# Optimization experiments

Measured on AMD Instinct MI355X. Metric: run time of the kernel, lower is better.

Reference implementation:

```python
import jax, jax.numpy as jnp
import numpy as np

B = 65536
HIDDEN = 200
K = 10          # num codewords == codeword dim (NearestEmbed(k, emb_size=k))
GROUPS = HIDDEN // K  # 20 sub-vectors of dim K per sample


def setup_inputs() -> dict:
    key = jax.random.key(0)
    ks = jax.random.split(key, 10)
    s = 0.05  # small init scale
    return {
        "x": jax.random.uniform(ks[0], (B, 784), dtype=jnp.float32),
        "W1": jax.random.normal(ks[1], (400, 784), dtype=jnp.float32) * s,
        "b1": jnp.zeros((400,), dtype=jnp.float32),
        "W2": jax.random.normal(ks[2], (HIDDEN, 400), dtype=jnp.float32) * s,
        "b2": jnp.zeros((HIDDEN,), dtype=jnp.float32),
        "W3": jax.random.normal(ks[3], (400, HIDDEN), dtype=jnp.float32) * s,
        "b3": jnp.zeros((400,), dtype=jnp.float32),
        "W4": jax.random.normal(ks[4], (784, 400), dtype=jnp.float32) * s,
        "b4": jnp.zeros((784,), dtype=jnp.float32),
        "codebook": jax.random.normal(ks[5], (K, K), dtype=jnp.float32),  # (n_codes, code_dim)
    }


def _quantize(z, codebook):
    # z: (B, K, GROUPS) -- quantize each length-K column vector to nearest codeword.
    v = jnp.transpose(z, (0, 2, 1))                       # (B, G, K)
    d2 = (jnp.sum(v * v, -1, keepdims=True)
          - 2.0 * jnp.einsum('bgk,ck->bgc', v, codebook)
          + jnp.sum(codebook * codebook, -1))             # (B, G, C)
    idx = jnp.argmin(d2, axis=-1)                         # (B, G)
    q = codebook[idx]                                     # (B, G, K) gather
    return jnp.transpose(q, (0, 2, 1)), idx               # (B, K, G)


def reference(x, W1, b1, W2, b2, W3, b3, W4, b4, codebook):
    # encode
    h1 = jax.nn.relu(x @ W1.T + b1)                       # (B, 400)
    z_e_flat = h1 @ W2.T + b2                             # (B, 200)
    z_e = z_e_flat.reshape(B, K, GROUPS)                  # (B, 10, 20)

    # z_q: straight-through quantization, codebook grad stopped (weight_sg=True)
    q, _ = _quantize(z_e, codebook)
    z_q = (z_e + jax.lax.stop_gradient(q - z_e)).reshape(B, HIDDEN)

    # emb: quantize detached z_e; gradient flows only to codebook via gather
    q2, _ = _quantize(jax.lax.stop_gradient(z_e), codebook)
    emb = q2.reshape(B, HIDDEN)

    # decode (original uses tanh on the output)
    h3 = jax.nn.relu(z_q @ W3.T + b3)                     # (B, 400)
    recon = jnp.tanh(h3 @ W4.T + b4)                      # (B, 784)
    return recon, z_e, emb
```

## Files before the change

### kernel.cpp

```cpp
#include <hip/hip_runtime.h>
#include <hip/hip_bf16.h>

#define NB   65536
#define KD   10
#define NG   20
#define NH   200
#define NH1  400
#define NIN  784

#define TAU 3e-4

using short8 = __attribute__((ext_vector_type(8))) short;
using f32x4  = __attribute__((ext_vector_type(4))) float;

__device__ inline float bf2f(unsigned short u) {
  union { unsigned int i; float f; } x; x.i = ((unsigned int)u) << 16; return x.f;
}
__device__ inline unsigned short f2bf(float v) {
  __hip_bfloat16 b = __float2bfloat16(v);
  return *reinterpret_cast<unsigned short*>(&b);
}
__device__ inline void split2(float v, unsigned short& h, unsigned short& l) {
  union { float f; unsigned int i; } u; u.f = v;
  const unsigned int hbits = u.i & 0xffff0000u;
  h = (unsigned short)(hbits >> 16);
  union { unsigned int i; float f; } w; w.i = hbits;
  l = f2bf(v - w.f);
}
__device__ inline void gload_lds16(const void* g, void* l) {
  __builtin_amdgcn_global_load_lds(
      (const __attribute__((address_space(1))) unsigned int*)g,
      (__attribute__((address_space(3))) unsigned int*)l, 16, 0, 0);
}

#define KSWZ(lane) ((((lane) & 3) ^ (((lane) >> 3) & 3)) * 8)
#define CSW(lane)  (((((lane) >> 4) ^ (((lane) >> 1) & 3))) * 8)

__global__ __launch_bounds__(512) void gemm1_fused(
    const float* __restrict__ xf,
    const unsigned short* __restrict__ Bhi, const unsigned short* __restrict__ Blo,
    const float* __restrict__ bias,
    unsigned short* __restrict__ Ohi, unsigned short* __restrict__ Olo)
{
  __shared__ __align__(16) short As_hi[2][128][32];
  __shared__ __align__(16) short As_lo[2][128][32];
  __shared__ __align__(16) short Bs_hi[2][128][32];
  __shared__ __align__(16) short Bs_lo[2][128][32];
  const int tid = threadIdx.x;
  const int lane = tid & 63, wid = tid >> 6;
  const int wr = wid >> 2, wc = wid & 3;
  const int bid = blockIdx.x;
  const int sw = (bid & 7) * 256 + (bid >> 3);
  const int n0 = (sw & 3) * 128;
  const int m0 = (sw >> 2) * 128;
  const int rr = lane >> 2;
  const int kswz = KSWZ(lane);
  const int csw = CSW(lane);
  const int fr = lane & 15;
  const int arow = tid >> 3;
  const int wbyte = ((tid & 7) * 8) ^ (((tid >> 4) & 3) << 4);
  const int acol = (tid & 7) * 4;

  f32x4 acc[4][2];
  #pragma unroll
  for (int i = 0; i < 4; ++i)
    #pragma unroll
    for (int j = 0; j < 2; ++j) acc[i][j] = (f32x4){0.f, 0.f, 0.f, 0.f};

  float4 va0, va1;

  auto loadA = [&](int ks) {
    const int k0 = ks * 32;
    const int kk = k0 + acol;
    va0 = make_float4(0.f, 0.f, 0.f, 0.f);
    va1 = va0;
    if (kk < NIN) {
      va0 = *reinterpret_cast<const float4*>(xf + (size_t)(m0 + arow) * NIN + kk);
      va1 = *reinterpret_cast<const float4*>(xf + (size_t)(m0 + 64 + arow) * NIN + kk);
    }
  };
  auto stageB = [&](int ks, int buf) {
    const int k0 = ks * 32;
    #pragma unroll
    for (int c = 0; c < 2; ++c) {
      const int ch = wid * 2 + c;
      if (ch < 8)
        gload_lds16(Bhi + (size_t)(n0 + ch * 16 + rr) * 800 + k0 + kswz,
                    (char*)&Bs_hi[buf][0][0] + ch * 1024);
      else
        gload_lds16(Blo + (size_t)(n0 + (ch - 8) * 16 + rr) * 800 + k0 + kswz,
                    (char*)&Bs_lo[buf][0][0] + (ch - 8) * 1024);
    }
  };
  auto writeA = [&](int buf) {
    char* bh = (char*)&As_hi[buf][0][0];
    char* bl = (char*)&As_lo[buf][0][0];
    short4 h, l;
    split2(va0.x, (unsigned short&)h.x, (unsigned short&)l.x);
    split2(va0.y, (unsigned short&)h.y, (unsigned short&)l.y);
    split2(va0.z, (unsigned short&)h.z, (unsigned short&)l.z);
    split2(va0.w, (unsigned short&)h.w, (unsigned short&)l.w);
    *reinterpret_cast<short4*>(bh + arow * 64 + wbyte) = h;
    *reinterpret_cast<short4*>(bl + arow * 64 + wbyte) = l;
    split2(va1.x, (unsigned short&)h.x, (unsigned short&)l.x);
    split2(va1.y, (unsigned short&)h.y, (unsigned short&)l.y);
    split2(va1.z, (unsigned short&)h.z, (unsigned short&)l.z);
    split2(va1.w, (unsigned short&)h.w, (unsigned short&)l.w);
    *reinterpret_cast<short4*>(bh + (64 + arow) * 64 + wbyte) = h;
    *reinterpret_cast<short4*>(bl + (64 + arow) * 64 + wbyte) = l;
  };

  stageB(0, 0);
  loadA(0);
  writeA(0);
  __syncthreads();

  for (int ks = 0; ks < 25; ++ks) {
    const int cur = ks & 1, nxt = cur ^ 1;
    const bool more = (ks + 1 < 25);
    if (more) {
      stageB(ks + 1, nxt);
      loadA(ks + 1);
    }
    short8 ah[4], al[4], bh[2], bl[2];
    #pragma unroll
    for (int i = 0; i < 4; ++i) {
      ah[i] = *reinterpret_cast<const short8*>(&As_hi[cur][wr * 64 + i * 16 + fr][csw]);
      al[i] = *reinterpret_cast<const short8*>(&As_lo[cur][wr * 64 + i * 16 + fr][csw]);
    }
    #pragma unroll
    for (int j = 0; j < 2; ++j) {
      bh[j] = *reinterpret_cast<const short8*>(&Bs_hi[cur][wc * 32 + j * 16 + fr][csw]);
      bl[j] = *reinterpret_cast<const short8*>(&Bs_lo[cur][wc * 32 + j * 16 + fr][csw]);
    }
    #pragma unroll
    for (int i = 0; i < 4; ++i)
      #pragma unroll
      for (int j = 0; j < 2; ++j) {
        acc[i][j] = __builtin_amdgcn_mfma_f32_16x16x32_bf16(ah[i], bh[j], acc[i][j], 0, 0, 0);
        acc[i][j] = __builtin_amdgcn_mfma_f32_16x16x32_bf16(al[i], bh[j], acc[i][j], 0, 0, 0);
        acc[i][j] = __builtin_amdgcn_mfma_f32_16x16x32_bf16(ah[i], bl[j], acc[i][j], 0, 0, 0);
      }
    if (more) writeA(nxt);
    __syncthreads();
  }

  #pragma unroll
  for (int j = 0; j < 2; ++j) {
    const int n = n0 + wc * 32 + j * 16 + (lane & 15);
    if (n >= NH1) continue;
    const float bn = bias[n];
    #pragma unroll
    for (int i = 0; i < 4; ++i) {
      const int mb = m0 + wr * 64 + i * 16 + (lane >> 4) * 4;
      #pragma unroll
      for (int r = 0; r < 4; ++r) {
        float v = fmaxf(acc[i][j][r] + bn, 0.f);
        unsigned short h, l;
        split2(v, h, l);
        Ohi[(size_t)(mb + r) * NH1 + n] = h;
        Olo[(size_t)(mb + r) * NH1 + n] = l;
      }
    }
  }
}

__global__ __launch_bounds__(256) void gemm2_split(
    const unsigned short* __restrict__ Ahi, const unsigned short* __restrict__ Alo,
    const unsigned short* __restrict__ Bhi, const unsigned short* __restrict__ Blo,
    const unsigned short* __restrict__ zp, const float* __restrict__ bias,
    float* __restrict__ Of)
{
  __shared__ __align__(16) short As_hi[128][32];
  __shared__ __align__(16) short As_lo[128][32];
  __shared__ __align__(16) short Bs_hi[128][32];
  __shared__ __align__(16) short Bs_lo[128][32];
  const int tid = threadIdx.x;
  const int lane = tid & 63, wid = tid >> 6;
  const int wr = wid >> 1, wc = wid & 1;
  const int bid = blockIdx.x;
  const int sw = (bid & 7) * 128 + (bid >> 3);
  const int n0 = (sw & 1) * 128;
  const int m0 = (sw >> 1) * 128;

  const unsigned short* G = (wid == 0) ? Ahi : (wid == 1) ? Alo
                          : (wid == 2) ? Bhi : Blo;
  short* Lt = (wid == 0) ? &As_hi[0][0] : (wid == 1) ? &As_lo[0][0]
            : (wid == 2) ? &Bs_hi[0][0] : &Bs_lo[0][0];
  const bool isA = wid < 2;
  const int rbase = isA ? m0 : n0;
  const int ld = isA ? 400 : 416;
  const int rr = lane >> 2;
  const int kswz = KSWZ(lane);
  const int csw = CSW(lane);

  f32x4 acc[4][4];
  #pragma unroll
  for (int i = 0; i < 4; ++i)
    #pragma unroll
    for (int j = 0; j < 4; ++j) acc[i][j] = (f32x4){0.f, 0.f, 0.f, 0.f};

  for (int ks = 0; ks < 13; ++ks) {
    const int k0 = ks * 32;
    #pragma unroll
    for (int c = 0; c < 8; ++c) {
      const unsigned short* src =
          G + (size_t)(rbase + c * 16 + rr) * ld + k0 + kswz;
      if (isA && (k0 + kswz >= 400)) src = zp;
      gload_lds16(src, (char*)Lt + c * 1024);
    }
    __syncthreads();
    short8 ah[4], al[4], bh[4], bl[4];
    #pragma unroll
    for (int i = 0; i < 4; ++i) {
      ah[i] = *reinterpret_cast<const short8*>(&As_hi[wr * 64 + i * 16 + (lane & 15)][csw]);
      al[i] = *reinterpret_cast<const short8*>(&As_lo[wr * 64 + i * 16 + (lane & 15)][csw]);
      bh[i] = *reinterpret_cast<const short8*>(&Bs_hi[wc * 64 + i * 16 + (lane & 15)][csw]);
      bl[i] = *reinterpret_cast<const short8*>(&Bs_lo[wc * 64 + i * 16 + (lane & 15)][csw]);
    }
    #pragma unroll
    for (int i = 0; i < 4; ++i)
      #pragma unroll
      for (int j = 0; j < 4; ++j) {
        acc[i][j] = __builtin_amdgcn_mfma_f32_16x16x32_bf16(ah[i], bh[j], acc[i][j], 0, 0, 0);
        acc[i][j] = __builtin_amdgcn_mfma_f32_16x16x32_bf16(al[i], bh[j], acc[i][j], 0, 0, 0);
        acc[i][j] = __builtin_amdgcn_mfma_f32_16x16x32_bf16(ah[i], bl[j], acc[i][j], 0, 0, 0);
      }
    __syncthreads();
  }

  #pragma unroll
  for (int j = 0; j < 4; ++j) {
    const int n = n0 + wc * 64 + j * 16 + (lane & 15);
    if (n >= NH) continue;
    const float bn = bias[n];
    #pragma unroll
    for (int i = 0; i < 4; ++i) {
      const int mb = m0 + wr * 64 + i * 16 + (lane >> 4) * 4;
      #pragma unroll
      for (int r = 0; r < 4; ++r)
        Of[(size_t)(mb + r) * NH + n] = acc[i][j][r] + bn;
    }
  }
}

__global__ __launch_bounds__(512) void gemm3_mfma(
    const unsigned short* __restrict__ A,
    const __hip_bfloat16* __restrict__ Bp,
    const float* __restrict__ bias, __hip_bfloat16* __restrict__ H3)
{
  __shared__ __align__(16) short As[2][128][32];
  __shared__ __align__(16) short Bs[2][128][32];
  const int tid = threadIdx.x;
  const int lane = tid & 63, wid = tid >> 6;
  const int wr = wid >> 2, wc = wid & 3;
  const int bid = blockIdx.x;
  const int sw = (bid & 7) * 256 + (bid >> 3);
  const int n0 = (sw & 3) * 128;
  const int m0 = (sw >> 2) * 128;
  const int rr = lane >> 2;
  const int kswz = KSWZ(lane);
  const int csw = CSW(lane);
  const int fr = lane & 15;
  const short* Ag = (const short*)A;
  const short* Bg = (const short*)Bp;

  f32x4 acc[4][2];
  #pragma unroll
  for (int i = 0; i < 4; ++i)
    #pragma unroll
    for (int j = 0; j < 2; ++j) acc[i][j] = (f32x4){0.f, 0.f, 0.f, 0.f};

  auto stage = [&](int ks, int buf) {
    const int k0 = ks * 32;
    #pragma unroll
    for (int c = 0; c < 2; ++c) {
      const int ch = wid * 2 + c;
      if (ch < 8)
        gload_lds16(Ag + (size_t)(m0 + ch * 16 + rr) * 200 + k0 + kswz,
                    (char*)&As[buf][0][0] + ch * 1024);
      else
        gload_lds16(Bg + (size_t)(n0 + (ch - 8) * 16 + rr) * 224 + k0 + kswz,
                    (char*)&Bs[buf][0][0] + (ch - 8) * 1024);
    }
  };

  stage(0, 0);
  __syncthreads();
  for (int ks = 0; ks < 7; ++ks) {
    const int cur = ks & 1;
    if (ks + 1 < 7) stage(ks + 1, cur ^ 1);
    short8 af[4], bf[2];
    #pragma unroll
    for (int i = 0; i < 4; ++i)
      af[i] = *reinterpret_cast<const short8*>(&As[cur][wr * 64 + i * 16 + fr][csw]);
    #pragma unroll
    for (int j = 0; j < 2; ++j)
      bf[j] = *reinterpret_cast<const short8*>(&Bs[cur][wc * 32 + j * 16 + fr][csw]);
    #pragma unroll
    for (int i = 0; i < 4; ++i)
      #pragma unroll
      for (int j = 0; j < 2; ++j)
        acc[i][j] = __builtin_amdgcn_mfma_f32_16x16x32_bf16(af[i], bf[j], acc[i][j], 0, 0, 0);
    __syncthreads();
  }

  #pragma unroll
  for (int j = 0; j < 2; ++j) {
    const int n = n0 + wc * 32 + j * 16 + (lane & 15);
    if (n >= NH1) continue;
    const float bn = bias[n];
    #pragma unroll
    for (int i = 0; i < 4; ++i) {
      const int mb = m0 + wr * 64 + i * 16 + (lane >> 4) * 4;
      #pragma unroll
      for (int r = 0; r < 4; ++r)
        H3[(size_t)(mb + r) * NH1 + n] = __float2bfloat16(fmaxf(acc[i][j][r] + bn, 0.f));
    }
  }
}

__global__ __launch_bounds__(512) void gemm5_mfma(
    const __hip_bfloat16* __restrict__ A,
    const __hip_bfloat16* __restrict__ Bp,
    const float* __restrict__ bias, float* __restrict__ C)
{
  __shared__ __align__(16) short As[2][128][32];
  __shared__ __align__(16) short Bs[2][128][32];
  const int tid = threadIdx.x;
  const int lane = tid & 63, wid = tid >> 6;
  const int wr = wid >> 2, wc = wid & 3;
  const int bid = blockIdx.x;
  const int sw = (bid & 7) * 448 + (bid >> 3);
  const int n0 = (sw % 7) * 128;
  const int m0 = (sw / 7) * 128;
  const int rr = lane >> 2;
  const int kswz = KSWZ(lane);
  const int csw = CSW(lane);
  const int fr = lane & 15;
  const short* Ag = (const short*)A;
  const short* Bg = (const short*)Bp;

  f32x4 acc[4][2];
  #pragma unroll
  for (int i = 0; i < 4; ++i)
    #pragma unroll
    for (int j = 0; j < 2; ++j) acc[i][j] = (f32x4){0.f, 0.f, 0.f, 0.f};

  auto stage = [&](int ks, int buf) {
    const int k0 = ks * 32;
    #pragma unroll
    for (int c = 0; c < 2; ++c) {
      const int ch = wid * 2 + c;
      if (ch < 8)
        gload_lds16(Ag + (size_t)(m0 + ch * 16 + rr) * 400 + k0 + kswz,
                    (char*)&As[buf][0][0] + ch * 1024);
      else
        gload_lds16(Bg + (size_t)(n0 + (ch - 8) * 16 + rr) * 416 + k0 + kswz,
                    (char*)&Bs[buf][0][0] + (ch - 8) * 1024);
    }
  };

  stage(0, 0);
  __syncthreads();
  for (int ks = 0; ks < 13; ++ks) {
    const int cur = ks & 1;
    if (ks + 1 < 13) stage(ks + 1, cur ^ 1);
    short8 af[4], bf[2];
    #pragma unroll
    for (int i = 0; i < 4; ++i)
      af[i] = *reinterpret_cast<const short8*>(&As[cur][wr * 64 + i * 16 + fr][csw]);
    #pragma unroll
    for (int j = 0; j < 2; ++j)
      bf[j] = *reinterpret_cast<const short8*>(&Bs[cur][wc * 32 + j * 16 + fr][csw]);
    #pragma unroll
    for (int i = 0; i < 4; ++i)
      #pragma unroll
      for (int j = 0; j < 2; ++j)
        acc[i][j] = __builtin_amdgcn_mfma_f32_16x16x32_bf16(af[i], bf[j], acc[i][j], 0, 0, 0);
    __syncthreads();
  }

  #pragma unroll
  for (int j = 0; j < 2; ++j) {
    const int n = n0 + wc * 32 + j * 16 + (lane & 15);
    if (n >= NIN) continue;
    const float bn = bias[n];
    #pragma unroll
    for (int i = 0; i < 4; ++i) {
      const int mb = m0 + wr * 64 + i * 16 + (lane >> 4) * 4;
      #pragma unroll
      for (int r = 0; r < 4; ++r) {
        const float zv = acc[i][j][r] + bn;
        const float t = __expf(2.0f * zv);
        C[(size_t)(mb + r) * NIN + n] = 1.0f - __fdividef(2.0f, t + 1.0f);
      }
    }
  }
}

__global__ __launch_bounds__(256) void prep_all(
    const float* __restrict__ W1, const float* __restrict__ W2,
    const float* __restrict__ W3, const float* __restrict__ W4,
    unsigned short* __restrict__ W1ph, unsigned short* __restrict__ W1pl,
    unsigned short* __restrict__ W2ph, unsigned short* __restrict__ W2pl,
    __hip_bfloat16* __restrict__ W3p, __hip_bfloat16* __restrict__ W4p)
{
  const int i = blockIdx.x * 256 + threadIdx.x;
  if (i < 409600) {
    const int n = i / 800, k = i % 800;
    const float v = (n < NH1 && k < NIN) ? W1[(size_t)n * NIN + k] : 0.f;
    unsigned short h, l; split2(v, h, l);
    W1ph[i] = h; W1pl[i] = l;
  } else if (i < 516096) {
    const int j = i - 409600;
    const int n = j / 416, k = j % 416;
    const float v = (n < NH && k < NH1) ? W2[(size_t)n * NH1 + k] : 0.f;
    unsigned short h, l; split2(v, h, l);
    W2ph[j] = h; W2pl[j] = l;
  } else if (i < 888832) {
    const int j = i - 516096;
    const int n = j / 416, k = j % 416;
    const float v = (n < NIN && k < NH1) ? W4[(size_t)n * NH1 + k] : 0.f;
    W4p[j] = __float2bfloat16(v);
  } else if (i < 1003520) {
    const int j = i - 888832;
    const int n = j / 224, k = j % 224;
    const float v = (n < NH1 && k < NH) ? W3[(size_t)n * NH + k] : 0.f;
    W3p[j] = __float2bfloat16(v);
  }
}

__global__ __launch_bounds__(256) void quant_kernel(
    const float* __restrict__ z_e, const float* __restrict__ cb,
    float* __restrict__ emb, unsigned short* __restrict__ ebf,
    unsigned int* __restrict__ sflag, int* __restrict__ scount,
    int* __restrict__ slist)
{
  __shared__ double cs[KD][KD];
  __shared__ double chalf[KD];
  __shared__ unsigned short cbf[KD][KD];
  const int tid = threadIdx.x;
  if (tid < KD * KD) {
    const double c = (double)cb[tid];
    cs[tid / KD][tid % KD] = c;
    cbf[tid / KD][tid % KD] = f2bf((float)c);
  }
  __syncthreads();
  if (tid < KD) {
    double s = 0.0;
    #pragma unroll
    for (int k = 0; k < KD; ++k) s += cs[tid][k] * cs[tid][k];
    chalf[tid] = 0.5 * s;
  }
  __syncthreads();

  const int gi = blockIdx.x * 256 + tid;
  const int b = gi / NG;
  const int g = gi % NG;
  const float* zrow = z_e + (size_t)b * NH + g;
  double v[KD];
  #pragma unroll
  for (int k = 0; k < KD; ++k) v[k] = (double)zrow[k * NG];

  int best = 0; double bt = 1e300, bt2 = 1e300;
  #pragma unroll
  for (int j = 0; j < KD; ++j) {
    double t = chalf[j];
    #pragma unroll
    for (int k = 0; k < KD; ++k) t -= v[k] * cs[j][k];
    if (t < bt) { bt2 = bt; bt = t; best = j; }
    else if (t < bt2) { bt2 = t; }
  }
  float* ep = emb + (size_t)b * NH + g;
  unsigned short* eb = ebf + (size_t)b * NH + g;
  #pragma unroll
  for (int k = 0; k < KD; ++k) {
    ep[k * NG] = (float)cs[best][k];
    eb[k * NG] = cbf[best][k];
  }
  if (bt2 - bt < TAU) {
    if (atomicExch(&sflag[b], 1u) == 0u)
      slist[atomicAdd(scount, 1)] = b;
  }
}

__global__ __launch_bounds__(256) void repair_kernel(
    const float* __restrict__ x, const float* __restrict__ W1,
    const float* __restrict__ b1, const float* __restrict__ W2,
    const float* __restrict__ b2, const float* __restrict__ cb,
    const int* __restrict__ slist, const int* __restrict__ scount,
    float* __restrict__ emb, unsigned short* __restrict__ ebf)
{
  __shared__ double h1s[NH1];
  __shared__ double zs[NH];
  __shared__ double cs[KD][KD];
  __shared__ double chalf[KD];
  const int tid = threadIdx.x;
  const int lane = tid & 63, wv = tid >> 6;
  if (tid < KD * KD) cs[tid / KD][tid % KD] = (double)cb[tid];
  __syncthreads();
  if (tid < KD) {
    double s = 0.0;
    #pragma unroll
    for (int k = 0; k < KD; ++k) s += cs[tid][k] * cs[tid][k];
    chalf[tid] = 0.5 * s;
  }

  int S = *scount; if (S > NB) S = NB;

  for (int si = blockIdx.x; si < S; si += gridDim.x) {
    const int b = slist[si];
    double xr[4][4];
    #pragma unroll
    for (int it = 0; it < 4; ++it) {
      const int c4 = it * 64 + lane;
      if (c4 < 196) {
        float4 v = reinterpret_cast<const float4*>(x + (size_t)b * NIN)[c4];
        xr[it][0] = v.x; xr[it][1] = v.y; xr[it][2] = v.z; xr[it][3] = v.w;
      } else {
        xr[it][0] = xr[it][1] = xr[it][2] = xr[it][3] = 0.0;
      }
    }
    for (int j = wv; j < NH1; j += 4) {
      const float4* wr = reinterpret_cast<const float4*>(W1 + (size_t)j * NIN);
      double s0 = 0, s1 = 0, s2 = 0, s3 = 0;
      #pragma unroll
      for (int it = 0; it < 4; ++it) {
        const int c4 = it * 64 + lane;
        if (c4 < 196) {
          float4 w = wr[c4];
          s0 = fma(xr[it][0], (double)w.x, s0);
          s1 = fma(xr[it][1], (double)w.y, s1);
          s2 = fma(xr[it][2], (double)w.z, s2);
          s3 = fma(xr[it][3], (double)w.w, s3);
        }
      }
      double s = (s0 + s1) + (s2 + s3);
      #pragma unroll
      for (int off = 32; off > 0; off >>= 1) s += __shfl_down(s, off);
      if (lane == 0) { double h = s + (double)b1[j]; h1s[j] = h > 0.0 ? h : 0.0; }
    }
    __syncthreads();
    double hr[2][4];
    #pragma unroll
    for (int it = 0; it < 2; ++it) {
      const int c4 = it * 64 + lane;
      if (c4 < 100) {
        hr[it][0] = h1s[4 * c4 + 0]; hr[it][1] = h1s[4 * c4 + 1];
        hr[it][2] = h1s[4 * c4 + 2]; hr[it][3] = h1s[4 * c4 + 3];
      } else {
        hr[it][0] = hr[it][1] = hr[it][2] = hr[it][3] = 0.0;
      }
    }
    for (int n = wv; n < NH; n += 4) {
      const float4* wr = reinterpret_cast<const float4*>(W2 + (size_t)n * NH1);
      double s0 = 0, s1 = 0, s2 = 0, s3 = 0;
      #pragma unroll
      for (int it = 0; it < 2; ++it) {
        const int c4 = it * 64 + lane;
        if (c4 < 100) {
          float4 w = wr[c4];
          s0 = fma(hr[it][0], (double)w.x, s0);
          s1 = fma(hr[it][1], (double)w.y, s1);
          s2 = fma(hr[it][2], (double)w.z, s2);
          s3 = fma(hr[it][3], (double)w.w, s3);
        }
      }
      double s = (s0 + s1) + (s2 + s3);
      #pragma unroll
      for (int off = 32; off > 0; off >>= 1) s += __shfl_down(s, off);
      if (lane == 0) zs[n] = s + (double)b2[n];
    }
    __syncthreads();
    if (tid < NG) {
      const int g = tid;
      int best = 0; double bt = 1e300;
      #pragma unroll
      for (int j = 0; j < KD; ++j) {
        double t = chalf[j];
        #pragma unroll
        for (int k = 0; k < KD; ++k) t -= zs[k * NG + g] * cs[j][k];
        if (t < bt) { bt = t; best = j; }
      }
      #pragma unroll
      for (int k = 0; k < KD; ++k) {
        const float cv = (float)cs[best][k];
        emb[(size_t)b * NH + k * NG + g] = cv;
        ebf[(size_t)b * NH + k * NG + g] = f2bf(cv);
      }
    }
    __syncthreads();
  }
}

extern "C" void kernel_launch(void* const* d_in, const int* in_sizes, int n_in,
                              void* d_out, int out_size, void* d_ws, size_t ws_size,
                              hipStream_t stream) {
  const float* x  = (const float*)d_in[0];
  const float* W1 = (const float*)d_in[1];
  const float* b1 = (const float*)d_in[2];
  const float* W2 = (const float*)d_in[3];
  const float* b2 = (const float*)d_in[4];
  const float* W3 = (const float*)d_in[5];
  const float* b3 = (const float*)d_in[6];
  const float* W4 = (const float*)d_in[7];
  const float* b4 = (const float*)d_in[8];
  const float* cb = (const float*)d_in[9];

  float* out   = (float*)d_out;
  float* recon = out;
  float* z_e   = out + (size_t)NB * NIN;
  float* emb   = z_e + (size_t)NB * NH;

  unsigned short* h1_lo  = (unsigned short*)emb;
  unsigned short* emb_bf = (unsigned short*)recon;

  char* ws = (char*)d_ws;
  int*            scount = (int*)ws;
  unsigned short* zp    = (unsigned short*)(ws + 256);
  unsigned int*   sflag = (unsigned int*)(ws + 4096);
  __hip_bfloat16* W3p   = (__hip_bfloat16*)(ws + (1u << 20));
  int*            slist = (int*)(ws + (4u << 20));
  __hip_bfloat16* W4p   = (__hip_bfloat16*)(ws + (6u << 20));
  unsigned short* W1ph  = (unsigned short*)(ws + (7u << 20));
  unsigned short* W1pl  = (unsigned short*)(ws + (9u << 20));
  unsigned short* W2ph  = (unsigned short*)(ws + (11u << 20));
  unsigned short* W2pl  = (unsigned short*)(ws + (12u << 20));
  unsigned short* h1_hi = (unsigned short*)(ws + (16u << 20));
  __hip_bfloat16* h3    = (__hip_bfloat16*)(ws + (16u << 20));

  dim3 blk(256);
  hipMemsetAsync(ws, 0, 4096 + NB * 4, stream);
  prep_all<<<3920, blk, 0, stream>>>(W1, W2, W3, W4, W1ph, W1pl, W2ph, W2pl, W3p, W4p);

  gemm1_fused<<<2048, dim3(512), 0, stream>>>(x, W1ph, W1pl, b1, h1_hi, h1_lo);
  gemm2_split<<<1024, blk, 0, stream>>>(h1_hi, h1_lo, W2ph, W2pl, zp, b2, z_e);

  quant_kernel<<<(NB * NG) / 256, blk, 0, stream>>>(z_e, cb, emb, emb_bf, sflag, scount, slist);
  repair_kernel<<<2048, blk, 0, stream>>>(x, W1, b1, W2, b2, cb, slist, scount, emb, emb_bf);

  gemm3_mfma<<<2048, dim3(512), 0, stream>>>(emb_bf, W3p, b3, h3);
  gemm5_mfma<<<3584, dim3(512), 0, stream>>>(h3, W4p, b4, recon);
}
```

Baseline: 560.4 us.

## Double-buffer gemm2 with 8 waves and stage quant inputs through LDS

```diff
diff --git a/kernel.cpp b/kernel.cpp
--- a/kernel.cpp
+++ b/kernel.cpp
@@ -165,63 +165,74 @@
   }
 }
 
-__global__ __launch_bounds__(256) void gemm2_split(
+__global__ __launch_bounds__(512) void gemm2_split(
     const unsigned short* __restrict__ Ahi, const unsigned short* __restrict__ Alo,
     const unsigned short* __restrict__ Bhi, const unsigned short* __restrict__ Blo,
     const unsigned short* __restrict__ zp, const float* __restrict__ bias,
     float* __restrict__ Of)
 {
-  __shared__ __align__(16) short As_hi[128][32];
-  __shared__ __align__(16) short As_lo[128][32];
-  __shared__ __align__(16) short Bs_hi[128][32];
-  __shared__ __align__(16) short Bs_lo[128][32];
+  __shared__ __align__(16) short As_hi[2][128][32];
+  __shared__ __align__(16) short As_lo[2][128][32];
+  __shared__ __align__(16) short Bs_hi[2][128][32];
+  __shared__ __align__(16) short Bs_lo[2][128][32];
   const int tid = threadIdx.x;
   const int lane = tid & 63, wid = tid >> 6;
-  const int wr = wid >> 1, wc = wid & 1;
+  const int wr = wid >> 2, wc = wid & 3;
   const int bid = blockIdx.x;
   const int sw = (bid & 7) * 128 + (bid >> 3);
   const int n0 = (sw & 1) * 128;
   const int m0 = (sw >> 1) * 128;
-
-  const unsigned short* G = (wid == 0) ? Ahi : (wid == 1) ? Alo
-                          : (wid == 2) ? Bhi : Blo;
-  short* Lt = (wid == 0) ? &As_hi[0][0] : (wid == 1) ? &As_lo[0][0]
-            : (wid == 2) ? &Bs_hi[0][0] : &Bs_lo[0][0];
-  const bool isA = wid < 2;
-  const int rbase = isA ? m0 : n0;
-  const int ld = isA ? 400 : 416;
   const int rr = lane >> 2;
   const int kswz = KSWZ(lane);
   const int csw = CSW(lane);
-
-  f32x4 acc[4][4];
+  const int fr = lane & 15;
+
+  f32x4 acc[4][2];
   #pragma unroll
   for (int i = 0; i < 4; ++i)
     #pragma unroll
-    for (int j = 0; j < 4; ++j) acc[i][j] = (f32x4){0.f, 0.f, 0.f, 0.f};
+    for (int j = 0; j < 2; ++j) acc[i][j] = (f32x4){0.f, 0.f, 0.f, 0.f};
+
+  auto stage = [&](int ks, int buf) {
+    const int k0 = ks * 32;
+    #pragma unroll
+    for (int q = 0; q < 4; ++q) {
+      const int c = wid * 4 + q;
+      const int tile = c >> 3, sub = c & 7;
+      const unsigned short* G;
+      char* Lt;
+      int rbase, ld;
+      if (tile == 0)      { G = Ahi; Lt = (char*)&As_hi[buf][0][0]; rbase = m0; ld = 400; }
+      else if (tile == 1) { G = Alo; Lt = (char*)&As_lo[buf][0][0]; rbase = m0; ld = 400; }
+      else if (tile == 2) { G = Bhi; Lt = (char*)&Bs_hi[buf][0][0]; rbase = n0; ld = 416; }
+      else                { G = Blo; Lt = (char*)&Bs_lo[buf][0][0]; rbase = n0; ld = 416; }
+      const unsigned short* src = G + (size_t)(rbase + sub * 16 + rr) * ld + k0 + kswz;
+      if (tile < 2 && (k0 + kswz >= 400)) src = zp;
+      gload_lds16(src, Lt + sub * 1024);
+    }
+  };
+
+  stage(0, 0);
+  __syncthreads();
 
   for (int ks = 0; ks < 13; ++ks) {
-    const int k0 = ks * 32;
-    #pragma unroll
-    for (int c = 0; c < 8; ++c) {
-      const unsigned short* src =
-          G + (size_t)(rbase + c * 16 + rr) * ld + k0 + kswz;
-      if (isA && (k0 + kswz >= 400)) src = zp;
-      gload_lds16(src, (char*)Lt + c * 1024);
-    }
-    __syncthreads();
-    short8 ah[4], al[4], bh[4], bl[4];
+    const int cur = ks & 1;
+    if (ks + 1 < 13) stage(ks + 1, cur ^ 1);
+    short8 ah[4], al[4], bh[2], bl[2];
     #pragma unroll
     for (int i = 0; i < 4; ++i) {
-      ah[i] = *reinterpret_cast<const short8*>(&As_hi[wr * 64 + i * 16 + (lane & 15)][csw]);
-      al[i] = *reinterpret_cast<const short8*>(&As_lo[wr * 64 + i * 16 + (lane & 15)][csw]);
-      bh[i] = *reinterpret_cast<const short8*>(&Bs_hi[wc * 64 + i * 16 + (lane & 15)][csw]);
-      bl[i] = *reinterpret_cast<const short8*>(&Bs_lo[wc * 64 + i * 16 + (lane & 15)][csw]);
+      ah[i] = *reinterpret_cast<const short8*>(&As_hi[cur][wr * 64 + i * 16 + fr][csw]);
+      al[i] = *reinterpret_cast<const short8*>(&As_lo[cur][wr * 64 + i * 16 + fr][csw]);
+    }
+    #pragma unroll
+    for (int j = 0; j < 2; ++j) {
+      bh[j] = *reinterpret_cast<const short8*>(&Bs_hi[cur][wc * 32 + j * 16 + fr][csw]);
+      bl[j] = *reinterpret_cast<const short8*>(&Bs_lo[cur][wc * 32 + j * 16 + fr][csw]);
     }
     #pragma unroll
     for (int i = 0; i < 4; ++i)
       #pragma unroll
-      for (int j = 0; j < 4; ++j) {
+      for (int j = 0; j < 2; ++j) {
         acc[i][j] = __builtin_amdgcn_mfma_f32_16x16x32_bf16(ah[i], bh[j], acc[i][j], 0, 0, 0);
         acc[i][j] = __builtin_amdgcn_mfma_f32_16x16x32_bf16(al[i], bh[j], acc[i][j], 0, 0, 0);
         acc[i][j] = __builtin_amdgcn_mfma_f32_16x16x32_bf16(ah[i], bl[j], acc[i][j], 0, 0, 0);
@@ -230,8 +241,8 @@
   }
 
   #pragma unroll
-  for (int j = 0; j < 4; ++j) {
-    const int n = n0 + wc * 64 + j * 16 + (lane & 15);
+  for (int j = 0; j < 2; ++j) {
+    const int n = n0 + wc * 32 + j * 16 + (lane & 15);
     if (n >= NH) continue;
     const float bn = bias[n];
     #pragma unroll
@@ -431,12 +442,13 @@
   }
 }
 
-__global__ __launch_bounds__(256) void quant_kernel(
+__global__ __launch_bounds__(320) void quant_kernel(
     const float* __restrict__ z_e, const float* __restrict__ cb,
     float* __restrict__ emb, unsigned short* __restrict__ ebf,
     unsigned int* __restrict__ sflag, int* __restrict__ scount,
     int* __restrict__ slist)
 {
+  __shared__ float zsl[16 * NH];
   __shared__ double cs[KD][KD];
   __shared__ double chalf[KD];
   __shared__ unsigned short cbf[KD][KD];
@@ -453,12 +465,16 @@
     for (int k = 0; k < KD; ++k) s += cs[tid][k] * cs[tid][k];
     chalf[tid] = 0.5 * s;
   }
+
+  const int b0 = blockIdx.x * 16;
+  for (int t = tid; t < 16 * NH; t += 320)
+    zsl[t] = z_e[(size_t)b0 * NH + t];
   __syncthreads();
 
-  const int gi = blockIdx.x * 256 + tid;
-  const int b = gi / NG;
-  const int g = gi % NG;
-  const float* zrow = z_e + (size_t)b * NH + g;
+  const int s16 = tid / NG;
+  const int g = tid % NG;
+  const int b = b0 + s16;
+  const float* zrow = &zsl[s16 * NH + g];
   double v[KD];
   #pragma unroll
   for (int k = 0; k < KD; ++k) v[k] = (double)zrow[k * NG];
@@ -635,9 +651,9 @@
   prep_all<<<3920, blk, 0, stream>>>(W1, W2, W3, W4, W1ph, W1pl, W2ph, W2pl, W3p, W4p);
 
   gemm1_fused<<<2048, dim3(512), 0, stream>>>(x, W1ph, W1pl, b1, h1_hi, h1_lo);
-  gemm2_split<<<1024, blk, 0, stream>>>(h1_hi, h1_lo, W2ph, W2pl, zp, b2, z_e);
-
-  quant_kernel<<<(NB * NG) / 256, blk, 0, stream>>>(z_e, cb, emb, emb_bf, sflag, scount, slist);
+  gemm2_split<<<1024, dim3(512), 0, stream>>>(h1_hi, h1_lo, W2ph, W2pl, zp, b2, z_e);
+
+  quant_kernel<<<NB / 16, dim3(320), 0, stream>>>(z_e, cb, emb, emb_bf, sflag, scount, slist);
   repair_kernel<<<2048, blk, 0, stream>>>(x, W1, b1, W2, b2, cb, slist, scount, emb, emb_bf);
 
   gemm3_mfma<<<2048, dim3(512), 0, stream>>>(emb_bf, W3p, b3, h3);
```

Result: no change. 564.7 us (+0.8%).
